# Performance work log

Hardware: AMD Instinct MI355X
Metric: run time of the kernel (lower is better)

The kernel has to match this reference:

```python
import jax, jax.numpy as jnp
import numpy as np
import math

EMBED_DIM = 1024
N_HEADS = 16
HEAD_DIM = EMBED_DIM // N_HEADS
B, N = 2, 2048


def setup_inputs() -> dict:
    key = jax.random.key(0)
    k1, k2, k3 = jax.random.split(key, 3)
    x = jax.random.normal(k1, (B, N, EMBED_DIM), dtype=jnp.float32)
    # Per-head Linear(D, 3*head_dim), stacked over heads. PyTorch Linear init scale ~1/sqrt(fan_in).
    bound = 1.0 / math.sqrt(EMBED_DIM)
    Wkqv = jax.random.uniform(k2, (N_HEADS, EMBED_DIM, 3 * HEAD_DIM), dtype=jnp.float32, minval=-bound, maxval=bound)
    bkqv = jax.random.uniform(k3, (N_HEADS, 3 * HEAD_DIM), dtype=jnp.float32, minval=-bound, maxval=bound)
    return {"x": x, "Wkqv": Wkqv, "bkqv": bkqv}


def reference(x, Wkqv, bkqv):
    Bx, Nx, D = x.shape
    hd = Wkqv.shape[-1] // 3
    # all heads at once: [B, H, N, 3*hd]
    proj = jnp.einsum('bnd,hdf->bhnf', x, Wkqv) + bkqv[None, :, None, :]
    # torch.split order in the original is (k, q, v)
    k, q, v = jnp.split(proj, 3, axis=-1)
    # scores = q @ k^T / sqrt(head_dim)   [B, H, N, N]
    scores = jnp.einsum('bhqd,bhkd->bhqk', q, k) / math.sqrt(hd)
    causal = jnp.tril(jnp.ones((Nx, Nx), dtype=bool))
    scores = jnp.where(causal[None, None, :, :], scores, -jnp.inf)
    attn = jax.nn.softmax(scores, axis=-1)
    out = jnp.einsum('bhqk,bhkd->bhqd', attn, v)  # [B, H, N, hd]
    # concat heads -> [B, N, D]  (forward() passes no out_matrix, so no output projection)
    return out.transpose(0, 2, 1, 3).reshape(Bx, Nx, D)
```

## Files before the change

### kernel.cpp

```cpp
#include <hip/hip_runtime.h>
#include <math.h>

typedef float f32x4 __attribute__((ext_vector_type(4)));
typedef __bf16 bf16x8 __attribute__((ext_vector_type(8)));

#define MFMA16(a, b, c) __builtin_amdgcn_mfma_f32_16x16x32_bf16((a), (b), (c), 0, 0, 0)

constexpr int Bsz = 2, Nseq = 2048, Dm = 1024, Hh = 16, HDim = 64, F3 = 192;
constexpr int Mrows = Bsz * Nseq;
constexpr int NC = Hh * F3;
constexpr float QSCALE = 0.125f * 1.4426950408889634f;

__device__ inline void load_lds16(const void* g, void* l) {
    __builtin_amdgcn_global_load_lds((const __attribute__((address_space(1))) void*)g,
                                     (__attribute__((address_space(3))) void*)l, 16, 0, 0);
}

__global__ __launch_bounds__(256) void conv_x_kernel(const float* __restrict__ x,
                                                     __bf16* __restrict__ xb) {
    int i = blockIdx.x * 256 + threadIdx.x;
    const float4* xv = reinterpret_cast<const float4*>(x);
    float4 a = xv[2 * i];
    float4 b = xv[2 * i + 1];
    bf16x8 o = {(__bf16)a.x, (__bf16)a.y, (__bf16)a.z, (__bf16)a.w,
                (__bf16)b.x, (__bf16)b.y, (__bf16)b.z, (__bf16)b.w};
    *reinterpret_cast<bf16x8*>(xb + 8 * i) = o;
}

__global__ __launch_bounds__(256) void conv_w_kernel(const float* __restrict__ w,
                                                     __bf16* __restrict__ wt) {
    __shared__ __bf16 tile[32][66];
    int h = blockIdx.z, d0 = blockIdx.x * 32, c0 = blockIdx.y * 64;
    for (int i = threadIdx.x; i < 32 * 64; i += 256) {
        int di = i >> 6, cj = i & 63;
        tile[di][cj] = (__bf16)w[(size_t)(h * Dm + d0 + di) * F3 + c0 + cj];
    }
    __syncthreads();
    for (int i = threadIdx.x; i < 32 * 64; i += 256) {
        int ci = i >> 5, dj = i & 31;
        wt[(size_t)(h * F3 + c0 + ci) * Dm + d0 + dj] = tile[dj][ci];
    }
}

__global__ __launch_bounds__(256) void gemm_proj(const __bf16* __restrict__ xb,
                                                 const __bf16* __restrict__ wt,
                                                 const float* __restrict__ bias,
                                                 __bf16* __restrict__ kbuf,
                                                 __bf16* __restrict__ qbuf,
                                                 __bf16* __restrict__ vt) {
    __shared__ __align__(16) __bf16 Ab[128 * 64];
    __shared__ __align__(16) __bf16 Bb[128 * 64];
    int wave = threadIdx.x >> 6, lane = threadIdx.x & 63;
    int col = lane & 15, quad = lane >> 4;
    int wm = wave & 1, wn = wave >> 1;
    int r0 = blockIdx.x * 128, n0 = blockIdx.y * 128;

    f32x4 acc[4][4] = {};

    for (int kt = 0; kt < Dm; kt += 64) {
        __syncthreads();
#pragma unroll
        for (int it = 0; it < 4; it++) {
            int row_t = it * 32 + wave * 8 + (lane >> 3);
            int jg = (lane & 7) ^ (row_t & 7);
            load_lds16(xb + (size_t)(r0 + row_t) * Dm + kt + jg * 8,
                       Ab + it * 2048 + wave * 512);
            load_lds16(wt + (size_t)(n0 + row_t) * Dm + kt + jg * 8,
                       Bb + it * 2048 + wave * 512);
        }
        __syncthreads();

#pragma unroll
        for (int ks = 0; ks < 2; ks++) {
            int cq = ks * 4 + quad;
            bf16x8 af[4], bfr[4];
#pragma unroll
            for (int mt = 0; mt < 4; mt++) {
                int row = wm * 64 + mt * 16 + col;
                af[mt] = *reinterpret_cast<const bf16x8*>(Ab + row * 64 + (cq ^ (row & 7)) * 8);
            }
#pragma unroll
            for (int nt = 0; nt < 4; nt++) {
                int row = wn * 64 + nt * 16 + col;
                bfr[nt] = *reinterpret_cast<const bf16x8*>(Bb + row * 64 + (cq ^ (row & 7)) * 8);
            }
#pragma unroll
            for (int mt = 0; mt < 4; mt++)
#pragma unroll
                for (int nt = 0; nt < 4; nt++)
                    acc[mt][nt] = MFMA16(af[mt], bfr[nt], acc[mt][nt]);
        }
    }

#pragma unroll
    for (int nt = 0; nt < 4; nt++) {
        int g = n0 + wn * 64 + nt * 16 + col;
        int h = g / F3, c = g - h * F3;
        float bv = bias[g];
        bool isq = (c >= 64 && c < 128), isv = (c >= 128);
        int cd = c & 63;
#pragma unroll
        for (int mt = 0; mt < 4; mt++) {
#pragma unroll
            for (int rg = 0; rg < 4; rg++) {
                int r = r0 + wm * 64 + mt * 16 + quad * 4 + rg;
                int b = r >> 11, n = r & (Nseq - 1);
                float v = acc[mt][nt][rg] + bv;
                if (isq) v *= QSCALE;
                size_t bh = (size_t)(b * Hh + h);
                if (isv) vt[(bh * HDim + cd) * Nseq + n] = (__bf16)v;
                else ((isq) ? qbuf : kbuf)[(bh * Nseq + n) * HDim + cd] = (__bf16)v;
            }
        }
    }
}

__global__ __launch_bounds__(256) void proj_small(const float* __restrict__ x,
                                                  const __bf16* __restrict__ wt,
                                                  const float* __restrict__ bias,
                                                  __bf16* __restrict__ kbuf,
                                                  __bf16* __restrict__ qbuf,
                                                  __bf16* __restrict__ vt) {
    int h = blockIdx.y;
    int wave = threadIdx.x >> 6, lane = threadIdx.x & 63;
    int col = lane & 15, quad = lane >> 4;
    int r0 = blockIdx.x * 128 + wave * 32;

    f32x4 acc[12][2] = {};
    const float* xr0 = x + (size_t)(r0 + col) * Dm + quad * 8;
    const float* xr1 = xr0 + 16 * Dm;
    const __bf16* wbase = wt + (size_t)(h * F3 + col) * Dm + quad * 8;

    for (int k0 = 0; k0 < Dm; k0 += 32) {
        float4 a0lo = *reinterpret_cast<const float4*>(xr0 + k0);
        float4 a0hi = *reinterpret_cast<const float4*>(xr0 + k0 + 4);
        float4 a1lo = *reinterpret_cast<const float4*>(xr1 + k0);
        float4 a1hi = *reinterpret_cast<const float4*>(xr1 + k0 + 4);
        bf16x8 a0 = {(__bf16)a0lo.x, (__bf16)a0lo.y, (__bf16)a0lo.z, (__bf16)a0lo.w,
                     (__bf16)a0hi.x, (__bf16)a0hi.y, (__bf16)a0hi.z, (__bf16)a0hi.w};
        bf16x8 a1 = {(__bf16)a1lo.x, (__bf16)a1lo.y, (__bf16)a1lo.z, (__bf16)a1lo.w,
                     (__bf16)a1hi.x, (__bf16)a1hi.y, (__bf16)a1hi.z, (__bf16)a1hi.w};
#pragma unroll
        for (int ct = 0; ct < 12; ct++) {
            bf16x8 bf = *reinterpret_cast<const bf16x8*>(wbase + ct * 16 * Dm + k0);
            acc[ct][0] = MFMA16(a0, bf, acc[ct][0]);
            acc[ct][1] = MFMA16(a1, bf, acc[ct][1]);
        }
    }
#pragma unroll
    for (int ct = 0; ct < 12; ct++) {
        int c = ct * 16 + col;
        float bv = bias[h * F3 + c];
        int cd = c & 63;
        bool isq = (c >= 64 && c < 128), isv = (c >= 128);
#pragma unroll
        for (int rt = 0; rt < 2; rt++) {
#pragma unroll
            for (int rg = 0; rg < 4; rg++) {
                int r = r0 + rt * 16 + quad * 4 + rg;
                int b = r >> 11, n = r & (Nseq - 1);
                float v = acc[ct][rt][rg] + bv;
                if (isq) v *= QSCALE;
                size_t bh = (size_t)(b * Hh + h);
                if (isv) vt[(bh * HDim + cd) * Nseq + n] = (__bf16)v;
                else ((isq) ? qbuf : kbuf)[(bh * Nseq + n) * HDim + cd] = (__bf16)v;
            }
        }
    }
}

__global__ __launch_bounds__(512) void attn_kernel(const __bf16* __restrict__ qbuf,
                                                   const __bf16* __restrict__ kbuf,
                                                   const __bf16* __restrict__ vt,
                                                   float* __restrict__ out) {
    __shared__ __align__(16) __bf16 Kb[64 * 64];
    __shared__ __align__(16) __bf16 Vb[64 * 64];
    __shared__ __align__(16) __bf16 plds[8][16][72];
    int bh = blockIdx.x;
    int b = bh >> 4, h = bh & 15;
    int pair = blockIdx.y;
    int wave = threadIdx.x >> 6, lane = threadIdx.x & 63;
    int col = lane & 15, quad = lane >> 4;
    int tile = (wave < 4) ? pair : (31 - pair);
    int q0 = tile * 64 + (wave & 3) * 16;

    const __bf16* qbase = qbuf + (size_t)bh * Nseq * HDim;
    const __bf16* kbase = kbuf + (size_t)bh * Nseq * HDim;
    const __bf16* vbase = vt + (size_t)bh * HDim * Nseq;

    bf16x8 aq0 = *reinterpret_cast<const bf16x8*>(qbase + (q0 + col) * HDim + quad * 8);
    bf16x8 aq1 = *reinterpret_cast<const bf16x8*>(qbase + (q0 + col) * HDim + quad * 8 + 32);

    f32x4 o[4] = {};
    float lsum[4] = {0.f, 0.f, 0.f, 0.f};

    int mb = q0 & ~63;
    int loop_end = 2048 - 64 * pair;

    int srow = threadIdx.x >> 3;
    int schunk = (threadIdx.x & 7) ^ (srow & 7);
    const __bf16* ksrc0 = kbase + srow * HDim + schunk * 8;
    const __bf16* vsrc0 = vbase + (size_t)srow * Nseq + schunk * 8;
    __bf16* kdst = Kb + wave * 512;
    __bf16* vdst = Vb + wave * 512;

    int sw0 = ((quad ^ (col & 7)) * 8);
    int sw1 = (((quad + 4) ^ (col & 7)) * 8);

    for (int kb = 0; kb < loop_end; kb += 64) {
        __syncthreads();
        load_lds16(ksrc0 + kb * HDim, kdst);
        load_lds16(vsrc0 + kb, vdst);
        __syncthreads();

        if (kb <= mb) {
            bool masked = (kb == mb);
            f32x4 z = {};
            f32x4 s[4];
#pragma unroll
            for (int g = 0; g < 4; g++) {
                const __bf16* krow = Kb + (col + 16 * g) * 64;
                bf16x8 k0 = *reinterpret_cast<const bf16x8*>(krow + sw0);
                bf16x8 k1 = *reinterpret_cast<const bf16x8*>(krow + sw1);
                s[g] = MFMA16(aq0, k0, z);
                s[g] = MFMA16(aq1, k1, s[g]);
            }
            if (masked) {
#pragma unroll
                for (int g = 0; g < 4; g++) {
#pragma unroll
                    for (int r = 0; r < 4; r++) {
                        int qi = q0 + quad * 4 + r;
                        float p = (kb + col + 16 * g <= qi) ? exp2f(s[g][r]) : 0.f;
                        lsum[r] += p;
                        plds[wave][quad * 4 + r][col + 16 * g] = (__bf16)p;
                    }
                }
            } else {
#pragma unroll
                for (int g = 0; g < 4; g++) {
#pragma unroll
                    for (int r = 0; r < 4; r++) {
                        float p = exp2f(s[g][r]);
                        lsum[r] += p;
                        plds[wave][quad * 4 + r][col + 16 * g] = (__bf16)p;
                    }
                }
            }
            bf16x8 pa0 = *reinterpret_cast<const bf16x8*>(&plds[wave][col][quad * 8]);
            bf16x8 pa1 = *reinterpret_cast<const bf16x8*>(&plds[wave][col][32 + quad * 8]);
#pragma unroll
            for (int nt = 0; nt < 4; nt++) {
                const __bf16* vrow = Vb + (col + 16 * nt) * 64;
                bf16x8 v0 = *reinterpret_cast<const bf16x8*>(vrow + sw0);
                bf16x8 v1 = *reinterpret_cast<const bf16x8*>(vrow + sw1);
                o[nt] = MFMA16(pa0, v0, o[nt]);
                o[nt] = MFMA16(pa1, v1, o[nt]);
            }
        }
    }

    float linv[4];
#pragma unroll
    for (int r = 0; r < 4; r++) {
        float s = lsum[r];
        s += __shfl_xor(s, 1);
        s += __shfl_xor(s, 2);
        s += __shfl_xor(s, 4);
        s += __shfl_xor(s, 8);
        linv[r] = 1.f / s;
    }
#pragma unroll
    for (int nt = 0; nt < 4; nt++) {
#pragma unroll
        for (int r = 0; r < 4; r++) {
            int qi = q0 + quad * 4 + r;
            out[((size_t)(b * Nseq + qi)) * Dm + h * HDim + nt * 16 + col] = o[nt][r] * linv[r];
        }
    }
}

extern "C" void kernel_launch(void* const* d_in, const int* in_sizes, int n_in,
                              void* d_out, int out_size, void* d_ws, size_t ws_size,
                              hipStream_t stream) {
    const float* x = nullptr;
    const float* w = nullptr;
    const float* bias = nullptr;
    for (int i = 0; i < n_in; i++) {
        if (in_sizes[i] == Mrows * Dm) x = (const float*)d_in[i];
        else if (in_sizes[i] == Hh * Dm * F3) w = (const float*)d_in[i];
        else if (in_sizes[i] == Hh * F3) bias = (const float*)d_in[i];
    }
    float* outp = (float*)d_out;

    char* ws = (char*)d_ws;
    __bf16* wt = (__bf16*)(ws);
    __bf16* kbuf = (__bf16*)(ws + 6291456);
    __bf16* qbuf = (__bf16*)(ws + 6291456 + 8388608);
    __bf16* vt = (__bf16*)(ws + 6291456 + 2 * 8388608);
    __bf16* xb = (__bf16*)(ws + 6291456 + 3 * 8388608);

    conv_w_kernel<<<dim3(Dm / 32, F3 / 64, Hh), 256, 0, stream>>>(w, wt);
    if (ws_size >= (size_t)(6291456 + 4 * 8388608)) {
        conv_x_kernel<<<Mrows * Dm / (8 * 256), 256, 0, stream>>>(x, xb);
        gemm_proj<<<dim3(Mrows / 128, NC / 128), 256, 0, stream>>>(xb, wt, bias, kbuf, qbuf, vt);
    } else {
        proj_small<<<dim3(Mrows / 128, Hh), 256, 0, stream>>>(x, wt, bias, kbuf, qbuf, vt);
    }
    attn_kernel<<<dim3(32, 16), 512, 0, stream>>>(qbuf, kbuf, vt, outp);
}
```

Measured before the change: 171.6 us.

## Retile projection GEMM to 256x256 with double-buffered async LDS loads

The projection GEMM moves from 128x128 tiles with 256 threads to 256x256 tiles with 512 threads. It double-buffers the LDS stages so global-to-LDS loads for tile k+2 overlap MFMA work on tile k, using vmcnt waits and raw barriers. It also remaps the block index with a swizzle for L2 locality and raises wave priority around the MFMA burst. The cost is much more LDS per block (128KB) and many more accumulator registers, so fewer blocks fit on each CU and the grid has only 192 blocks.

```diff
diff --git a/kernel.cpp b/kernel.cpp
--- a/kernel.cpp
+++ b/kernel.cpp
@@ -42,54 +42,79 @@
     }
 }
 
-__global__ __launch_bounds__(256) void gemm_proj(const __bf16* __restrict__ xb,
-                                                 const __bf16* __restrict__ wt,
-                                                 const float* __restrict__ bias,
-                                                 __bf16* __restrict__ kbuf,
-                                                 __bf16* __restrict__ qbuf,
-                                                 __bf16* __restrict__ vt) {
-    __shared__ __align__(16) __bf16 Ab[128 * 64];
-    __shared__ __align__(16) __bf16 Bb[128 * 64];
-    int wave = threadIdx.x >> 6, lane = threadIdx.x & 63;
+__global__ __launch_bounds__(512, 2) void gemm_proj(const __bf16* __restrict__ xb,
+                                                    const __bf16* __restrict__ wt,
+                                                    const float* __restrict__ bias,
+                                                    __bf16* __restrict__ kbuf,
+                                                    __bf16* __restrict__ qbuf,
+                                                    __bf16* __restrict__ vt) {
+    __shared__ __align__(16) __bf16 Ab[2][256 * 64];
+    __shared__ __align__(16) __bf16 Bb[2][256 * 64];
+
+    int flat = blockIdx.x;
+    int swz = (flat & 7) * 24 + (flat >> 3);
+    int bm = swz / 12, bn = swz % 12;
+    int r0 = bm * 256, n0 = bn * 256;
+
+    int w = threadIdx.x >> 6, lane = threadIdx.x & 63;
     int col = lane & 15, quad = lane >> 4;
-    int wm = wave & 1, wn = wave >> 1;
-    int r0 = blockIdx.x * 128, n0 = blockIdx.y * 128;
-
-    f32x4 acc[4][4] = {};
-
-    for (int kt = 0; kt < Dm; kt += 64) {
-        __syncthreads();
-#pragma unroll
-        for (int it = 0; it < 4; it++) {
-            int row_t = it * 32 + wave * 8 + (lane >> 3);
-            int jg = (lane & 7) ^ (row_t & 7);
-            load_lds16(xb + (size_t)(r0 + row_t) * Dm + kt + jg * 8,
-                       Ab + it * 2048 + wave * 512);
-            load_lds16(wt + (size_t)(n0 + row_t) * Dm + kt + jg * 8,
-                       Bb + it * 2048 + wave * 512);
-        }
-        __syncthreads();
+    int wm = w >> 2, wn = w & 3;
+
+    f32x4 acc[8][4] = {};
+
+    auto stage = [&](int kt, int s) {
+        int rbase = w * 32;
+        int rl = lane >> 3;
+        int cg = ((lane & 7) ^ rl) * 8;
+#pragma unroll
+        for (int i = 0; i < 4; i++) {
+            int row = rbase + i * 8 + rl;
+            load_lds16(xb + (size_t)(r0 + row) * Dm + kt * 64 + cg,
+                       &Ab[s][(rbase + i * 8) * 64]);
+            load_lds16(wt + (size_t)(n0 + row) * Dm + kt * 64 + cg,
+                       &Bb[s][(rbase + i * 8) * 64]);
+        }
+    };
+
+    stage(0, 0);
+    stage(1, 1);
+
+    for (int j = 0; j < 16; j++) {
+        int s = j & 1;
+        if (j < 15) asm volatile("s_waitcnt vmcnt(8)" ::: "memory");
+        else        asm volatile("s_waitcnt vmcnt(0)" ::: "memory");
+        __builtin_amdgcn_s_barrier();
+        asm volatile("" ::: "memory");
 
 #pragma unroll
         for (int ks = 0; ks < 2; ks++) {
             int cq = ks * 4 + quad;
-            bf16x8 af[4], bfr[4];
-#pragma unroll
-            for (int mt = 0; mt < 4; mt++) {
-                int row = wm * 64 + mt * 16 + col;
-                af[mt] = *reinterpret_cast<const bf16x8*>(Ab + row * 64 + (cq ^ (row & 7)) * 8);
+            bf16x8 af[8], bfr[4];
+#pragma unroll
+            for (int mt = 0; mt < 8; mt++) {
+                int row = wm * 128 + mt * 16 + col;
+                af[mt] = *reinterpret_cast<const bf16x8*>(
+                    &Ab[s][row * 64 + ((cq ^ (row & 7)) * 8)]);
             }
 #pragma unroll
             for (int nt = 0; nt < 4; nt++) {
                 int row = wn * 64 + nt * 16 + col;
-                bfr[nt] = *reinterpret_cast<const bf16x8*>(Bb + row * 64 + (cq ^ (row & 7)) * 8);
-            }
-#pragma unroll
-            for (int mt = 0; mt < 4; mt++)
+                bfr[nt] = *reinterpret_cast<const bf16x8*>(
+                    &Bb[s][row * 64 + ((cq ^ (row & 7)) * 8)]);
+            }
+            __builtin_amdgcn_s_setprio(1);
+#pragma unroll
+            for (int mt = 0; mt < 8; mt++)
 #pragma unroll
                 for (int nt = 0; nt < 4; nt++)
                     acc[mt][nt] = MFMA16(af[mt], bfr[nt], acc[mt][nt]);
-        }
+            __builtin_amdgcn_s_setprio(0);
+        }
+
+        asm volatile("" ::: "memory");
+        __builtin_amdgcn_s_barrier();
+        asm volatile("" ::: "memory");
+        if (j + 2 < 16) stage(j + 2, s);
     }
 
 #pragma unroll
@@ -100,10 +125,10 @@
         bool isq = (c >= 64 && c < 128), isv = (c >= 128);
         int cd = c & 63;
 #pragma unroll
-        for (int mt = 0; mt < 4; mt++) {
+        for (int mt = 0; mt < 8; mt++) {
 #pragma unroll
             for (int rg = 0; rg < 4; rg++) {
-                int r = r0 + wm * 64 + mt * 16 + quad * 4 + rg;
+                int r = r0 + wm * 128 + mt * 16 + quad * 4 + rg;
                 int b = r >> 11, n = r & (Nseq - 1);
                 float v = acc[mt][nt][rg] + bv;
                 if (isq) v *= QSCALE;
@@ -303,7 +328,7 @@
     conv_w_kernel<<<dim3(Dm / 32, F3 / 64, Hh), 256, 0, stream>>>(w, wt);
     if (ws_size >= (size_t)(6291456 + 4 * 8388608)) {
         conv_x_kernel<<<Mrows * Dm / (8 * 256), 256, 0, stream>>>(x, xb);
-        gemm_proj<<<dim3(Mrows / 128, NC / 128), 256, 0, stream>>>(xb, wt, bias, kbuf, qbuf, vt);
+        gemm_proj<<<dim3(Mrows / 256 * (NC / 256)), 512, 0, stream>>>(xb, wt, bias, kbuf, qbuf, vt);
     } else {
         proj_small<<<dim3(Mrows / 128, Hh), 256, 0, stream>>>(x, wt, bias, kbuf, qbuf, vt);
     }
```

New measurement: 169.6 us. Within noise of the previous version (-1.2%).
